# Kernel tuning notes

Hardware: AMD Instinct MI355X
Metric: run time of the kernel (lower is better)

Reference implementation:

```python
import jax, jax.numpy as jnp
import numpy as np

N = 100000   # nodes
E = 3200000  # directed edges (avg degree 32)
T = 2048     # total flattened orders across all moves
M = 256      # number of moves (segments)


def _gat(x, src, dst, Wl, bl, Wr, br, att, b):
    # GATv2Conv (heads=1, eval mode -> attention dropout off), with self loops
    xl = x @ Wl.T + bl              # [N,10]
    xr = x @ Wr.T + br              # [N,10]
    sl = jnp.arange(N)
    s = jnp.concatenate([src, sl])
    d = jnp.concatenate([dst, sl])
    e = jax.nn.leaky_relu(xl[s] + xr[d], 0.2) @ att    # [E+N]
    emax = jax.ops.segment_max(e, d, num_segments=N)
    ex = jnp.exp(e - emax[d])
    den = jax.ops.segment_sum(ex, d, num_segments=N)
    return jax.ops.segment_sum((ex / den[d])[:, None] * xl[s], d, num_segments=N) + b


def setup_inputs() -> dict:
    key = jax.random.key(0)
    ks = iter(jax.random.split(key, 64))
    rn = lambda shape, s=0.1: jax.random.normal(next(ks), shape, jnp.float32) * s
    inp = {}
    inp['x1'] = rn((N, 15), 1.0)
    inp['x2'] = rn((1, 4), 1.0)
    src = jax.random.randint(next(ks), (E,), 0, N, jnp.int32)
    off = jax.random.randint(next(ks), (E,), 1, N, jnp.int32)
    inp['edge_src'] = src
    inp['edge_dst'] = ((src + off) % N).astype(jnp.int32)
    inp['move_type'] = jax.random.randint(next(ks), (T,), 0, 2, jnp.int32)
    inp['m_src'] = jax.random.randint(next(ks), (T,), 0, N, jnp.int32)
    inp['m_dst'] = jax.random.randint(next(ks), (T,), 0, N, jnp.int32)
    inp['m_target'] = jax.random.randint(next(ks), (T,), 0, N, jnp.int32)
    inp['m_armies'] = jax.random.uniform(next(ks), (T,), jnp.float32) * 10.0
    inp['move_id'] = (jnp.arange(T, dtype=jnp.int32) // (T // M))  # sorted, all segments non-empty
    # GATv2 layer params (in dims 15, 25, 25 -> out 10)
    for i, din in [(1, 15), (2, 25), (3, 25)]:
        inp[f'Wl{i}'] = rn((10, din)); inp[f'bl{i}'] = rn((10,))
        inp[f'Wr{i}'] = rn((10, din)); inp[f'br{i}'] = rn((10,))
        inp[f'att{i}'] = rn((10,));   inp[f'bias{i}'] = rn((10,))
    inp['lin_W'] = rn((15, 29)); inp['lin_b'] = rn((15,))
    inp['lin2_W'] = rn((1, 15)); inp['lin2_b'] = rn((1,))
    inp['aaa_W'] = rn((20, 48)); inp['aaa_b'] = rn((20,))
    inp['ccc_W'] = rn((20, 23)); inp['ccc_b'] = rn((20,))
    inp['attl_W'] = rn((1, 20)); inp['attl_b'] = rn((1,))
    inp['pi_W'] = rn((1, 20));   inp['pi_b'] = rn((1,))
    return inp


def reference(x1, x2, edge_src, edge_dst, move_type, m_src, m_dst, m_target, m_armies, move_id,
              Wl1, bl1, Wr1, br1, att1, bias1,
              Wl2, bl2, Wr2, br2, att2, bias2,
              Wl3, bl3, Wr3, br3, att3, bias3,
              lin_W, lin_b, lin2_W, lin2_b, aaa_W, aaa_b, ccc_W, ccc_b,
              attl_W, attl_b, pi_W, pi_b):
    h = jax.nn.relu(_gat(x1, edge_src, edge_dst, Wl1, bl1, Wr1, br1, att1, bias1))
    h = jax.nn.relu(_gat(jnp.concatenate([h, x1], 1), edge_src, edge_dst, Wl2, bl2, Wr2, br2, att2, bias2))
    x = jax.nn.relu(_gat(jnp.concatenate([h, x1], 1), edge_src, edge_dst, Wl3, bl3, Wr3, br3, att3, bias3))

    # per-order features (both branches computed, selected by move_type)
    extra = (0.6 * m_armies - 0.7 * (x1[m_dst, 3] + x1[m_dst, 4]))[:, None]
    feat_a = jnp.concatenate([x[m_src], x[m_dst], x1[m_src, 3:], x1[m_dst, 1:], m_armies[:, None], extra], axis=1)  # [T,48]
    a_out = jax.nn.relu(feat_a @ aaa_W.T + aaa_b)
    feat_d = jnp.concatenate([x[m_target], x1[m_target, 3:], m_armies[:, None]], axis=1)  # [T,23]
    d_out = jax.nn.relu(feat_d @ ccc_W.T + ccc_b)
    hm = jnp.where((move_type == 0)[:, None], a_out, d_out)  # [T,20]

    al = (hm @ attl_W.T + attl_b)[:, 0]   # [T]
    pi = (hm @ pi_W.T + pi_b)[:, 0]       # [T]
    amax = jax.ops.segment_max(al, move_id, num_segments=M)
    ex = jnp.exp(al - amax[move_id])
    den = jax.ops.segment_sum(ex, move_id, num_segments=M)
    p = jax.ops.segment_sum(ex / den[move_id] * pi, move_id, num_segments=M)  # [M]
    logp = jax.nn.log_softmax(p)

    x2t = jnp.tile(x2, (N, 1))
    v = jax.nn.relu(jnp.concatenate([x, x1, x2t], 1) @ lin_W.T + lin_b)
    V = jnp.tanh(jnp.mean(v @ lin2_W.T + lin2_b))
    return (V, logp)
```

## Files before the change

### kernel.cpp

```cpp
#include <hip/hip_runtime.h>
#include <cmath>

#define NN 100000
#define NE 3200000
#define TT 2048
#define MM 256
#define STR 16
#define HSTR 16
#define BSZ 64
#define NB 1563
#define EPB 16384
#define NBLK 196
#define SCAP 3072
#define PCAP 4096
#define CMAX 12
#define SRTP_CAP 5500000

__device__ __forceinline__ void atomicMaxF(float* addr, float v) {
    if (v >= 0.f) atomicMax((int*)addr, __float_as_int(v));
    else          atomicMin((unsigned int*)addr, __float_as_uint(v));
}

__device__ __forceinline__ unsigned short f2bf(float x) {
    unsigned u = __float_as_uint(x);
    u += 0x7FFFu + ((u >> 16) & 1u);
    return (unsigned short)(u >> 16);
}

__device__ __forceinline__ void unpack10(uint4 q, unsigned q2, float* a) {
    a[0] = __uint_as_float(q.x << 16);
    a[1] = __uint_as_float(q.x & 0xFFFF0000u);
    a[2] = __uint_as_float(q.y << 16);
    a[3] = __uint_as_float(q.y & 0xFFFF0000u);
    a[4] = __uint_as_float(q.z << 16);
    a[5] = __uint_as_float(q.z & 0xFFFF0000u);
    a[6] = __uint_as_float(q.w << 16);
    a[7] = __uint_as_float(q.w & 0xFFFF0000u);
    a[8] = __uint_as_float(q2 << 16);
    a[9] = __uint_as_float(q2 & 0xFFFF0000u);
}

__global__ __launch_bounds__(1024) void init_kernel(int* bcounts, int* pcounts, float* amax,
                                                    float* den_m, float* num_m, float* Vsum) {
    int i = blockIdx.x * 1024 + threadIdx.x;
    if (i < NB) { bcounts[i] = 0; pcounts[i] = 0; }
    if (i < MM) { amax[i] = -INFINITY; den_m[i] = 0.f; num_m[i] = 0.f; }
    if (i == 0) Vsum[0] = 0.f;
}

__global__ __launch_bounds__(256) void hist_kernel(const int* __restrict__ dst,
                                                   int* __restrict__ bcounts,
                                                   int* __restrict__ pcounts) {
    __shared__ int h[NB];
    int tid = threadIdx.x;
    for (int i = tid; i < NB; i += 256) h[i] = 0;
    __syncthreads();
    int base = blockIdx.x * EPB;
    int end = base + EPB; if (end > NE) end = NE;
    for (int i = base + tid * 4; i < end; i += 1024) {
        int4 d4 = *(const int4*)(dst + i);
        atomicAdd(&h[d4.x >> 6], 1);
        atomicAdd(&h[d4.y >> 6], 1);
        atomicAdd(&h[d4.z >> 6], 1);
        atomicAdd(&h[d4.w >> 6], 1);
    }
    __syncthreads();
    for (int i = tid; i < NB; i += 256) {
        int n = h[i];
        if (n) {
            atomicAdd(&bcounts[i], n);
            atomicAdd(&pcounts[i], (n + 15) & ~15);
        }
    }
}

__global__ __launch_bounds__(1024) void scan_kernel(const int* __restrict__ bcounts,
                                                    const int* __restrict__ pcounts,
                                                    int* __restrict__ bstart,
                                                    int* __restrict__ pbstart,
                                                    int* __restrict__ pcursor) {
    __shared__ int ssum[1024];
    __shared__ int psum[1024];
    int tid = threadIdx.x;
    const int per = (NB + 1023) / 1024;
    int base = tid * per;
    int s = 0, p = 0;
    for (int i = 0; i < per; i++) {
        int idx = base + i;
        if (idx < NB) { s += bcounts[idx]; p += pcounts[idx]; }
    }
    ssum[tid] = s; psum[tid] = p;
    __syncthreads();
    for (int off = 1; off < 1024; off <<= 1) {
        int v = (tid >= off) ? ssum[tid - off] : 0;
        int w = (tid >= off) ? psum[tid - off] : 0;
        __syncthreads();
        ssum[tid] += v; psum[tid] += w;
        __syncthreads();
    }
    int run = ssum[tid] - s;
    int prun = psum[tid] - p;
    for (int i = 0; i < per; i++) {
        int idx = base + i;
        if (idx < NB) {
            bstart[idx] = run;              run += bcounts[idx];
            pbstart[idx] = prun;
            pcursor[idx] = prun;            prun += pcounts[idx];
        }
    }
    if (tid == 0) { bstart[NB] = NE; pbstart[NB] = psum[1023]; }
}

__global__ __launch_bounds__(256) void scatter_kernel(const int* __restrict__ src,
                                                      const int* __restrict__ dst,
                                                      int* __restrict__ pcursor,
                                                      int* __restrict__ srtp) {
    __shared__ int h[NB];
    __shared__ int c[NB];
    int tid = threadIdx.x;
    for (int i = tid; i < NB; i += 256) h[i] = 0;
    __syncthreads();
    int base = blockIdx.x * EPB;
    int end = base + EPB; if (end > NE) end = NE;
    for (int i = base + tid * 4; i < end; i += 1024) {
        int4 d4 = *(const int4*)(dst + i);
        atomicAdd(&h[d4.x >> 6], 1);
        atomicAdd(&h[d4.y >> 6], 1);
        atomicAdd(&h[d4.z >> 6], 1);
        atomicAdd(&h[d4.w >> 6], 1);
    }
    __syncthreads();
    for (int i = tid; i < NB; i += 256) {
        int n = h[i];
        h[i] = n ? atomicAdd(&pcursor[i], (n + 15) & ~15) : 0;
        c[i] = 0;
    }
    __syncthreads();
    for (int i = base + tid * 4; i < end; i += 1024) {
        int4 d4 = *(const int4*)(dst + i);
        int4 s4 = *(const int4*)(src + i);
        int d, b, off;
        d = d4.x; b = d >> 6; off = atomicAdd(&c[b], 1); srtp[h[b] + off] = ((d & 63) << 17) | s4.x;
        d = d4.y; b = d >> 6; off = atomicAdd(&c[b], 1); srtp[h[b] + off] = ((d & 63) << 17) | s4.y;
        d = d4.z; b = d >> 6; off = atomicAdd(&c[b], 1); srtp[h[b] + off] = ((d & 63) << 17) | s4.z;
        d = d4.w; b = d >> 6; off = atomicAdd(&c[b], 1); srtp[h[b] + off] = ((d & 63) << 17) | s4.w;
    }
    __syncthreads();
    for (int i = tid; i < NB; i += 256) {
        int n = c[i];
        if (n) {
            int pad = (16 - (n & 15)) & 15;
            int baseo = h[i] + n;
            for (int k = 0; k < pad; k++) srtp[baseo + k] = -1;
        }
    }
}

__global__ __launch_bounds__(256) void sort2_kernel(const int* __restrict__ srtp,
                                                    const int* __restrict__ pbstart,
                                                    const int* __restrict__ bstart,
                                                    int* __restrict__ srt) {
    __shared__ int ent[PCAP];
    __shared__ int ent2[SCAP];
    __shared__ int cnts[BSZ];
    __shared__ int curs[BSZ];
    int b = blockIdx.x, tid = threadIdx.x;
    int p0 = pbstart[b], p1 = pbstart[b + 1];
    int pcnt = p1 - p0;
    if (pcnt > PCAP) pcnt = PCAP;
    if (tid < BSZ) cnts[tid] = 0;
    __syncthreads();
    for (int i = tid; i < pcnt; i += 256) {
        int p = srtp[p0 + i];
        ent[i] = p;
        if (p >= 0) atomicAdd(&cnts[p >> 17], 1);
    }
    __syncthreads();
    if (tid == 0) {
        int run = 0;
        for (int k = 0; k < BSZ; k++) { curs[k] = run; run += cnts[k]; }
    }
    __syncthreads();
    for (int i = tid; i < pcnt; i += 256) {
        int p = ent[i];
        if (p >= 0) {
            int pos = atomicAdd(&curs[p >> 17], 1);
            ent2[pos] = p;
        }
    }
    __syncthreads();
    int i0 = bstart[b];
    int cnt = bstart[b + 1] - i0;
    for (int i = tid; i < cnt; i += 256) srt[i0 + i] = ent2[i];
}

__global__ __launch_bounds__(256) void prep_kernel(
    const float* __restrict__ hprev,
    const float* __restrict__ x1,
    const float* __restrict__ Wl, const float* __restrict__ bl,
    const float* __restrict__ Wr, const float* __restrict__ br,
    unsigned short* __restrict__ xlh,
    unsigned short* __restrict__ xrh,
    int din)
{
    __shared__ float sWl[250], sWr[250], sbl[10], sbr[10];
    int tid = threadIdx.x;
    int nw = 10 * din;
    for (int i = tid; i < nw; i += blockDim.x) { sWl[i] = Wl[i]; sWr[i] = Wr[i]; }
    if (tid < 10) { sbl[tid] = bl[tid]; sbr[tid] = br[tid]; }
    __syncthreads();
    int n = blockIdx.x * blockDim.x + tid;
    if (n >= NN) return;

    float in[25];
    if (din == 15) {
        #pragma unroll
        for (int k = 0; k < 15; k++) in[k] = x1[n * 15 + k];
    } else {
        #pragma unroll
        for (int k = 0; k < 10; k++) in[k] = hprev[n * STR + k];
        #pragma unroll
        for (int k = 0; k < 15; k++) in[10 + k] = x1[n * 15 + k];
    }

    float slv[10], srv[10];
    #pragma unroll
    for (int j = 0; j < 10; j++) {
        float sl = sbl[j], sr = sbr[j];
        for (int k = 0; k < din; k++) {
            sl += in[k] * sWl[j * din + k];
            sr += in[k] * sWr[j * din + k];
        }
        slv[j] = sl; srv[j] = sr;
    }
    unsigned* lp = (unsigned*)(xlh + n * HSTR);
    unsigned* rp = (unsigned*)(xrh + n * HSTR);
    #pragma unroll
    for (int j = 0; j < 5; j++) {
        lp[j] = (unsigned)f2bf(slv[2 * j]) | ((unsigned)f2bf(slv[2 * j + 1]) << 16);
        rp[j] = (unsigned)f2bf(srv[2 * j]) | ((unsigned)f2bf(srv[2 * j + 1]) << 16);
    }
}

__global__ __launch_bounds__(256, 4) void gather_kernel(
    const int* __restrict__ srt, const int* __restrict__ bstart,
    const unsigned short* __restrict__ xlh, const unsigned short* __restrict__ xrh,
    const float* __restrict__ att, const float* __restrict__ bias,
    float* __restrict__ hout)
{
    __shared__ float accs[BSZ * 11];
    __shared__ float xrs[BSZ * 11];
    __shared__ float sat[10];
    int b = blockIdx.x, tid = threadIdx.x;
    if (tid < 10) sat[tid] = att[tid];
    __syncthreads();

    int n0 = b * BSZ;
    if (tid < BSZ) {
        int n = n0 + tid;
        if (n < NN) {
            const unsigned short* lr = xlh + n * HSTR;
            const unsigned short* rr = xrh + n * HSTR;
            uint4 ql = *(const uint4*)lr;  unsigned ql2 = *(const unsigned*)(lr + 8);
            uint4 qr = *(const uint4*)rr;  unsigned qr2 = *(const unsigned*)(rr + 8);
            float a[10], r[10];
            unpack10(ql, ql2, a);
            unpack10(qr, qr2, r);
            #pragma unroll
            for (int k = 0; k < 10; k++) xrs[tid * 11 + k] = r[k];
            float e = 0.f;
            #pragma unroll
            for (int k = 0; k < 10; k++) {
                float t = a[k] + r[k];
                t = t > 0.f ? t : 0.2f * t;
                e += sat[k] * t;
            }
            float ex = __expf(e);
            #pragma unroll
            for (int k = 0; k < 10; k++) accs[tid * 11 + k] = ex * a[k];
            accs[tid * 11 + 10] = ex;
        } else {
            #pragma unroll
            for (int k = 0; k < 11; k++) { accs[tid * 11 + k] = 0.f; xrs[tid * 11 + k] = 0.f; }
        }
    }
    __syncthreads();

    int i0 = bstart[b], i1 = bstart[b + 1];
    int cnt = i1 - i0;
    int C = (cnt + 255) >> 8;
    int a0 = i0 + tid * C;
    int a1 = a0 + C; if (a1 > i1) a1 = i1;
    int len = a1 - a0; if (len < 0) len = 0;
    if (len > 0) {
        int ps[CMAX];
        #pragma unroll
        for (int i = 0; i < CMAX; i++) ps[i] = (i < len) ? srt[a0 + i] : -1;

        const unsigned short* row0 = xlh + (ps[0] & 0x1FFFF) * HSTR;
        uint4 q = *(const uint4*)row0;
        unsigned q2 = *(const unsigned*)(row0 + 8);
        int cur = ps[0] >> 17;
        float racc[10];
        #pragma unroll
        for (int k = 0; k < 10; k++) racc[k] = 0.f;
        float rden = 0.f;
        #pragma unroll
        for (int i = 0; i < CMAX; i++) {
            if (i >= len) break;
            uint4 qn = q; unsigned q2n = q2;
            if (i + 1 < len) {
                const unsigned short* rn = xlh + (ps[i + 1] & 0x1FFFF) * HSTR;
                qn = *(const uint4*)rn;
                q2n = *(const unsigned*)(rn + 8);
            }
            int ld = ps[i] >> 17;
            if (ld != cur) {
                float* ac = accs + cur * 11;
                #pragma unroll
                for (int k = 0; k < 10; k++) atomicAdd(ac + k, racc[k]);
                atomicAdd(ac + 10, rden);
                #pragma unroll
                for (int k = 0; k < 10; k++) racc[k] = 0.f;
                rden = 0.f;
                cur = ld;
            }
            float a[10];
            unpack10(q, q2, a);
            const float* r = xrs + ld * 11;
            float e = 0.f;
            #pragma unroll
            for (int k = 0; k < 10; k++) {
                float t = a[k] + r[k];
                t = t > 0.f ? t : 0.2f * t;
                e += sat[k] * t;
            }
            float ex = __expf(e);
            rden += ex;
            #pragma unroll
            for (int k = 0; k < 10; k++) racc[k] += ex * a[k];
            q = qn; q2 = q2n;
        }
        float* ac = accs + cur * 11;
        #pragma unroll
        for (int k = 0; k < 10; k++) atomicAdd(ac + k, racc[k]);
        atomicAdd(ac + 10, rden);
    }
    __syncthreads();

    if (tid < BSZ) {
        int n = n0 + tid;
        if (n < NN) {
            float inv = 1.f / accs[tid * 11 + 10];
            #pragma unroll
            for (int k = 0; k < 10; k++) {
                float v = accs[tid * 11 + k] * inv + bias[k];
                hout[n * STR + k] = v > 0.f ? v : 0.f;
            }
        }
    }
}

__global__ __launch_bounds__(256) void value_kernel(
    const float* __restrict__ x, const float* __restrict__ x1, const float* __restrict__ x2,
    const float* __restrict__ lin_W, const float* __restrict__ lin_b,
    const float* __restrict__ lin2_W, const float* __restrict__ lin2_b,
    float* __restrict__ Vsum)
{
    __shared__ float sW[15 * 29], sb[15], sW2[15];
    __shared__ float red[256];
    int tid = threadIdx.x;
    for (int i = tid; i < 15 * 29; i += 256) sW[i] = lin_W[i];
    if (tid < 15) { sb[tid] = lin_b[tid]; sW2[tid] = lin2_W[tid]; }
    __syncthreads();
    int n = blockIdx.x * 256 + tid;
    float local = 0.f;
    if (n < NN) {
        float in[29];
        #pragma unroll
        for (int k = 0; k < 10; k++) in[k] = x[n * STR + k];
        #pragma unroll
        for (int k = 0; k < 15; k++) in[10 + k] = x1[n * 15 + k];
        #pragma unroll
        for (int k = 0; k < 4; k++) in[25 + k] = x2[k];
        float sc = lin2_b[0];
        #pragma unroll
        for (int j = 0; j < 15; j++) {
            float s = sb[j];
            for (int k = 0; k < 29; k++) s += in[k] * sW[j * 29 + k];
            sc += (s > 0.f ? s : 0.f) * sW2[j];
        }
        local = sc;
    }
    red[tid] = local;
    __syncthreads();
    for (int off = 128; off > 0; off >>= 1) {
        if (tid < off) red[tid] += red[tid + off];
        __syncthreads();
    }
    if (tid == 0) atomicAdd(Vsum, red[0]);
}

__global__ __launch_bounds__(256) void orders_kernel(
    const float* __restrict__ x, const float* __restrict__ x1,
    const int* __restrict__ move_type, const int* __restrict__ m_src,
    const int* __restrict__ m_dst, const int* __restrict__ m_target,
    const float* __restrict__ m_armies, const int* __restrict__ move_id,
    const float* __restrict__ aaa_W, const float* __restrict__ aaa_b,
    const float* __restrict__ ccc_W, const float* __restrict__ ccc_b,
    const float* __restrict__ attl_W, const float* __restrict__ attl_b,
    const float* __restrict__ pi_W, const float* __restrict__ pi_b,
    float* __restrict__ al_out, float* __restrict__ pi_out, float* __restrict__ amax)
{
    __shared__ float sA[20 * 48], sC[20 * 23], sAb[20], sCb[20];
    int tid = threadIdx.x;
    for (int i = tid; i < 20 * 48; i += 256) sA[i] = aaa_W[i];
    for (int i = tid; i < 20 * 23; i += 256) sC[i] = ccc_W[i];
    if (tid < 20) { sAb[tid] = aaa_b[tid]; sCb[tid] = ccc_b[tid]; }
    __syncthreads();
    int t = blockIdx.x * 256 + tid;
    if (t >= TT) return;

    float armies = m_armies[t];
    float hm[20];
    if (move_type[t] == 0) {
        int sn = m_src[t], dn = m_dst[t];
        float f[48];
        #pragma unroll
        for (int k = 0; k < 10; k++) f[k] = x[sn * STR + k];
        #pragma unroll
        for (int k = 0; k < 10; k++) f[10 + k] = x[dn * STR + k];
        #pragma unroll
        for (int k = 0; k < 12; k++) f[20 + k] = x1[sn * 15 + 3 + k];
        #pragma unroll
        for (int k = 0; k < 14; k++) f[32 + k] = x1[dn * 15 + 1 + k];
        f[46] = armies;
        f[47] = 0.6f * armies - 0.7f * (x1[dn * 15 + 3] + x1[dn * 15 + 4]);
        #pragma unroll
        for (int j = 0; j < 20; j++) {
            float s = sAb[j];
            for (int k = 0; k < 48; k++) s += f[k] * sA[j * 48 + k];
            hm[j] = s > 0.f ? s : 0.f;
        }
    } else {
        int tg = m_target[t];
        float f[23];
        #pragma unroll
        for (int k = 0; k < 10; k++) f[k] = x[tg * STR + k];
        #pragma unroll
        for (int k = 0; k < 12; k++) f[10 + k] = x1[tg * 15 + 3 + k];
        f[22] = armies;
        #pragma unroll
        for (int j = 0; j < 20; j++) {
            float s = sCb[j];
            for (int k = 0; k < 23; k++) s += f[k] * sC[j * 23 + k];
            hm[j] = s > 0.f ? s : 0.f;
        }
    }
    float a = attl_b[0], p = pi_b[0];
    #pragma unroll
    for (int j = 0; j < 20; j++) { a += hm[j] * attl_W[j]; p += hm[j] * pi_W[j]; }
    al_out[t] = a;
    pi_out[t] = p;
    atomicMaxF(&amax[move_id[t]], a);
}

__global__ __launch_bounds__(256) void orders2_kernel(
    const float* __restrict__ al, const float* __restrict__ piv,
    const int* __restrict__ move_id, const float* __restrict__ amax,
    float* __restrict__ den_m, float* __restrict__ num_m)
{
    int t = blockIdx.x * 256 + threadIdx.x;
    if (t >= TT) return;
    int m = move_id[t];
    float ex = __expf(al[t] - amax[m]);
    atomicAdd(den_m + m, ex);
    atomicAdd(num_m + m, ex * piv[t]);
}

__global__ __launch_bounds__(256) void final_kernel(
    const float* __restrict__ num_m, const float* __restrict__ den_m,
    const float* __restrict__ Vsum, float* __restrict__ out)
{
    __shared__ float sh[256];
    __shared__ float s_max, s_sum;
    int m = threadIdx.x;
    float p = num_m[m] / den_m[m];
    sh[m] = p;
    __syncthreads();
    for (int off = 128; off > 0; off >>= 1) {
        if (m < off) sh[m] = fmaxf(sh[m], sh[m + off]);
        __syncthreads();
    }
    if (m == 0) s_max = sh[0];
    __syncthreads();
    float e = __expf(p - s_max);
    sh[m] = e;
    __syncthreads();
    for (int off = 128; off > 0; off >>= 1) {
        if (m < off) sh[m] += sh[m + off];
        __syncthreads();
    }
    if (m == 0) s_sum = sh[0];
    __syncthreads();
    out[1 + m] = p - s_max - logf(s_sum);
    if (m == 0) out[0] = tanhf(Vsum[0] / (float)NN);
}

extern "C" void kernel_launch(void* const* d_in, const int* in_sizes, int n_in,
                              void* d_out, int out_size, void* d_ws, size_t ws_size,
                              hipStream_t stream) {
    const float* x1        = (const float*)d_in[0];
    const float* x2        = (const float*)d_in[1];
    const int*   esrc      = (const int*)d_in[2];
    const int*   edst      = (const int*)d_in[3];
    const int*   move_type = (const int*)d_in[4];
    const int*   m_src     = (const int*)d_in[5];
    const int*   m_dst     = (const int*)d_in[6];
    const int*   m_target  = (const int*)d_in[7];
    const float* m_armies  = (const float*)d_in[8];
    const int*   move_id   = (const int*)d_in[9];
    const float* W[3][6];
    for (int l = 0; l < 3; l++)
        for (int j = 0; j < 6; j++)
            W[l][j] = (const float*)d_in[10 + l * 6 + j];
    const float* lin_W  = (const float*)d_in[28];
    const float* lin_b  = (const float*)d_in[29];
    const float* lin2_W = (const float*)d_in[30];
    const float* lin2_b = (const float*)d_in[31];
    const float* aaa_W  = (const float*)d_in[32];
    const float* aaa_b  = (const float*)d_in[33];
    const float* ccc_W  = (const float*)d_in[34];
    const float* ccc_b  = (const float*)d_in[35];
    const float* attl_W = (const float*)d_in[36];
    const float* attl_b = (const float*)d_in[37];
    const float* pi_W   = (const float*)d_in[38];
    const float* pi_b   = (const float*)d_in[39];

    float* ws = (float*)d_ws;
    float* hA    = ws; ws += NN * STR;
    float* al    = ws; ws += TT;
    float* piv   = ws; ws += TT;
    float* amax  = ws; ws += MM;
    float* den_m = ws; ws += MM;
    float* num_m = ws; ws += MM;
    float* Vsum  = ws; ws += 1;
    unsigned short* xlh = (unsigned short*)ws; ws += NN * HSTR / 2;
    unsigned short* xrh = (unsigned short*)ws; ws += NN * HSTR / 2;
    int* iws = (int*)ws;
    int* bcounts = iws; iws += NB;
    int* pcounts = iws; iws += NB;
    int* bstart  = iws; iws += NB + 1;
    int* pbstart = iws; iws += NB + 1;
    int* pcursor = iws; iws += NB;
    int* srt     = iws; iws += NE;
    int* srtp    = iws; iws += SRTP_CAP;

    dim3 blk(256);
    dim3 gN((NN + 255) / 256);
    dim3 gT(TT / 256);

    init_kernel<<<dim3(2), dim3(1024), 0, stream>>>(bcounts, pcounts, amax, den_m, num_m, Vsum);
    hist_kernel<<<dim3(NBLK), blk, 0, stream>>>(edst, bcounts, pcounts);
    scan_kernel<<<dim3(1), dim3(1024), 0, stream>>>(bcounts, pcounts, bstart, pbstart, pcursor);
    scatter_kernel<<<dim3(NBLK), blk, 0, stream>>>(esrc, edst, pcursor, srtp);
    sort2_kernel<<<dim3(NB), blk, 0, stream>>>(srtp, pbstart, bstart, srt);

    prep_kernel<<<gN, blk, 0, stream>>>(nullptr, x1, W[0][0], W[0][1], W[0][2], W[0][3], xlh, xrh, 15);
    gather_kernel<<<dim3(NB), blk, 0, stream>>>(srt, bstart, xlh, xrh, W[0][4], W[0][5], hA);

    prep_kernel<<<gN, blk, 0, stream>>>(hA, x1, W[1][0], W[1][1], W[1][2], W[1][3], xlh, xrh, 25);
    gather_kernel<<<dim3(NB), blk, 0, stream>>>(srt, bstart, xlh, xrh, W[1][4], W[1][5], hA);

    prep_kernel<<<gN, blk, 0, stream>>>(hA, x1, W[2][0], W[2][1], W[2][2], W[2][3], xlh, xrh, 25);
    gather_kernel<<<dim3(NB), blk, 0, stream>>>(srt, bstart, xlh, xrh, W[2][4], W[2][5], hA);

    value_kernel<<<gN, blk, 0, stream>>>(hA, x1, x2, lin_W, lin_b, lin2_W, lin2_b, Vsum);
    orders_kernel<<<gT, blk, 0, stream>>>(hA, x1, move_type, m_src, m_dst, m_target,
                                          m_armies, move_id, aaa_W, aaa_b, ccc_W, ccc_b,
                                          attl_W, attl_b, pi_W, pi_b, al, piv, amax);
    orders2_kernel<<<gT, blk, 0, stream>>>(al, piv, move_id, amax, den_m, num_m);
    final_kernel<<<dim3(1), blk, 0, stream>>>(num_m, den_m, Vsum, (float*)d_out);
}
```

Baseline: 464.4 us.

## Stage scatter entries in LDS and write bucket runs with vectorized stores

The scatter kernel now does a local counting sort of its 16K edges in shared memory, via a block-wide prefix scan over bucket counts. It then writes each bucket's entries, padded to a multiple of 16, to global memory as contiguous int4 stores. Before, each edge went out as its own scattered 4-byte global write and the padding was a separate loop. The block also grows to 512 threads and uses about 84KB of LDS, which limits occupancy and adds a scan step.

```diff
diff --git a/kernel.cpp b/kernel.cpp
--- a/kernel.cpp
+++ b/kernel.cpp
@@ -111,47 +111,75 @@
     if (tid == 0) { bstart[NB] = NE; pbstart[NB] = psum[1023]; }
 }
 
-__global__ __launch_bounds__(256) void scatter_kernel(const int* __restrict__ src,
+__global__ __launch_bounds__(512) void scatter_kernel(const int* __restrict__ src,
                                                       const int* __restrict__ dst,
                                                       int* __restrict__ pcursor,
                                                       int* __restrict__ srtp) {
-    __shared__ int h[NB];
-    __shared__ int c[NB];
+    __shared__ int ent[EPB];
+    __shared__ int cnt[NB];
+    __shared__ int cur[NB];
+    __shared__ int gbase[NB];
+    __shared__ int psc[512];
     int tid = threadIdx.x;
-    for (int i = tid; i < NB; i += 256) h[i] = 0;
+    for (int i = tid; i < NB; i += 512) cnt[i] = 0;
     __syncthreads();
     int base = blockIdx.x * EPB;
     int end = base + EPB; if (end > NE) end = NE;
-    for (int i = base + tid * 4; i < end; i += 1024) {
+    for (int i = base + tid * 4; i < end; i += 2048) {
         int4 d4 = *(const int4*)(dst + i);
-        atomicAdd(&h[d4.x >> 6], 1);
-        atomicAdd(&h[d4.y >> 6], 1);
-        atomicAdd(&h[d4.z >> 6], 1);
-        atomicAdd(&h[d4.w >> 6], 1);
-    }
-    __syncthreads();
-    for (int i = tid; i < NB; i += 256) {
-        int n = h[i];
-        h[i] = n ? atomicAdd(&pcursor[i], (n + 15) & ~15) : 0;
-        c[i] = 0;
-    }
-    __syncthreads();
-    for (int i = base + tid * 4; i < end; i += 1024) {
+        atomicAdd(&cnt[d4.x >> 6], 1);
+        atomicAdd(&cnt[d4.y >> 6], 1);
+        atomicAdd(&cnt[d4.z >> 6], 1);
+        atomicAdd(&cnt[d4.w >> 6], 1);
+    }
+    __syncthreads();
+    const int PT = (NB + 511) / 512;
+    int t0 = tid * PT;
+    int s = 0;
+    #pragma unroll
+    for (int j = 0; j < PT; j++) { int idx = t0 + j; if (idx < NB) s += cnt[idx]; }
+    psc[tid] = s;
+    __syncthreads();
+    for (int off = 1; off < 512; off <<= 1) {
+        int v = (tid >= off) ? psc[tid - off] : 0;
+        __syncthreads();
+        psc[tid] += v;
+        __syncthreads();
+    }
+    int run = psc[tid] - s;
+    #pragma unroll
+    for (int j = 0; j < PT; j++) {
+        int idx = t0 + j;
+        if (idx < NB) { cur[idx] = run; run += cnt[idx]; }
+    }
+    for (int b = tid; b < NB; b += 512) {
+        int n = cnt[b];
+        gbase[b] = n ? atomicAdd(&pcursor[b], (n + 15) & ~15) : 0;
+    }
+    __syncthreads();
+    for (int i = base + tid * 4; i < end; i += 2048) {
         int4 d4 = *(const int4*)(dst + i);
         int4 s4 = *(const int4*)(src + i);
         int d, b, off;
-        d = d4.x; b = d >> 6; off = atomicAdd(&c[b], 1); srtp[h[b] + off] = ((d & 63) << 17) | s4.x;
-        d = d4.y; b = d >> 6; off = atomicAdd(&c[b], 1); srtp[h[b] + off] = ((d & 63) << 17) | s4.y;
-        d = d4.z; b = d >> 6; off = atomicAdd(&c[b], 1); srtp[h[b] + off] = ((d & 63) << 17) | s4.z;
-        d = d4.w; b = d >> 6; off = atomicAdd(&c[b], 1); srtp[h[b] + off] = ((d & 63) << 17) | s4.w;
-    }
-    __syncthreads();
-    for (int i = tid; i < NB; i += 256) {
-        int n = c[i];
-        if (n) {
-            int pad = (16 - (n & 15)) & 15;
-            int baseo = h[i] + n;
-            for (int k = 0; k < pad; k++) srtp[baseo + k] = -1;
+        d = d4.x; b = d >> 6; off = atomicAdd(&cur[b], 1); ent[off] = ((d & 63) << 17) | s4.x;
+        d = d4.y; b = d >> 6; off = atomicAdd(&cur[b], 1); ent[off] = ((d & 63) << 17) | s4.y;
+        d = d4.z; b = d >> 6; off = atomicAdd(&cur[b], 1); ent[off] = ((d & 63) << 17) | s4.z;
+        d = d4.w; b = d >> 6; off = atomicAdd(&cur[b], 1); ent[off] = ((d & 63) << 17) | s4.w;
+    }
+    __syncthreads();
+    for (int b = tid; b < NB; b += 512) {
+        int n = cnt[b];
+        if (!n) continue;
+        int lb = cur[b] - n;
+        int gb = gbase[b];
+        int p16 = (n + 15) & ~15;
+        for (int k = 0; k < p16; k += 4) {
+            int4 v;
+            v.x = (k + 0 < n) ? ent[lb + k + 0] : -1;
+            v.y = (k + 1 < n) ? ent[lb + k + 1] : -1;
+            v.z = (k + 2 < n) ? ent[lb + k + 2] : -1;
+            v.w = (k + 3 < n) ? ent[lb + k + 3] : -1;
+            *(int4*)(srtp + gb + k) = v;
         }
     }
 }
@@ -563,7 +591,7 @@
     init_kernel<<<dim3(2), dim3(1024), 0, stream>>>(bcounts, pcounts, amax, den_m, num_m, Vsum);
     hist_kernel<<<dim3(NBLK), blk, 0, stream>>>(edst, bcounts, pcounts);
     scan_kernel<<<dim3(1), dim3(1024), 0, stream>>>(bcounts, pcounts, bstart, pbstart, pcursor);
-    scatter_kernel<<<dim3(NBLK), blk, 0, stream>>>(esrc, edst, pcursor, srtp);
+    scatter_kernel<<<dim3(NBLK), dim3(512), 0, stream>>>(esrc, edst, pcursor, srtp);
     sort2_kernel<<<dim3(NB), blk, 0, stream>>>(srtp, pbstart, bstart, srt);
 
     prep_kernel<<<gN, blk, 0, stream>>>(nullptr, x1, W[0][0], W[0][1], W[0][2], W[0][3], xlh, xrh, 15);
```

After: 441.4 us. -5.0%, faster.
